# Kernel tuning notes

Measured on AMD Instinct MI355X. Metric: run time of the kernel, lower is better.

The kernel has to match this reference:

```python
import jax, jax.numpy as jnp
import numpy as np

B, T, C, H = 2, 2048, 2048, 16
HS = C // H
EPS = 1e-5


def _ln(x, w, b):
    mu = jnp.mean(x, axis=-1, keepdims=True)
    var = jnp.mean(jnp.square(x - mu), axis=-1, keepdims=True)
    return (x - mu) * jax.lax.rsqrt(var + EPS) * w + b


def setup_inputs() -> dict:
    key = jax.random.key(0)
    ks = jax.random.split(key, 8)
    s = 0.02
    return {
        "x": jax.random.normal(ks[0], (B, T, C), jnp.float32),
        "ln1_w": jnp.ones((C,), jnp.float32),
        "ln1_b": jnp.zeros((C,), jnp.float32),
        "w_qkv": jax.random.normal(ks[1], (C, 3 * C), jnp.float32) * s,
        "b_qkv": jnp.zeros((3 * C,), jnp.float32),
        "w_proj": jax.random.normal(ks[2], (C, C), jnp.float32) * s,
        "b_proj": jnp.zeros((C,), jnp.float32),
        "ln2_w": jnp.ones((C,), jnp.float32),
        "ln2_b": jnp.zeros((C,), jnp.float32),
        "w_fc": jax.random.normal(ks[3], (C, 4 * C), jnp.float32) * s,
        "b_fc": jnp.zeros((4 * C,), jnp.float32),
        "w_fc2": jax.random.normal(ks[4], (4 * C, C), jnp.float32) * s,
        "b_fc2": jnp.zeros((C,), jnp.float32),
    }


def reference(x, ln1_w, ln1_b, w_qkv, b_qkv, w_proj, b_proj,
              ln2_w, ln2_b, w_fc, b_fc, w_fc2, b_fc2):
    # --- attention branch (kv_cache=None -> L=0, burst=False, no padding mask) ---
    h = _ln(x, ln1_w, ln1_b)
    qkv = h @ w_qkv + b_qkv  # (B, T, 3C)
    q, k, v = jnp.split(qkv, 3, axis=-1)
    q = q.reshape(B, T, H, HS).transpose(0, 2, 1, 3)  # (B, H, T, HS)
    k = k.reshape(B, T, H, HS).transpose(0, 2, 1, 3)
    v = v.reshape(B, T, H, HS).transpose(0, 2, 1, 3)
    att = jnp.einsum('bhqd,bhkd->bhqk', q, k) * (1.0 / np.sqrt(HS))
    causal = jnp.tril(jnp.ones((T, T), bool))  # bias[0:T, 0:T]
    att = jnp.where(causal, att, -jnp.inf)
    att = jax.nn.softmax(att, axis=-1)
    y = jnp.einsum('bhqk,bhkd->bhqd', att, v)
    y = y.transpose(0, 2, 1, 3).reshape(B, T, C)
    y = y @ w_proj + b_proj
    x = x + y
    # --- MLP branch ---
    h = _ln(x, ln2_w, ln2_b)
    h = jax.nn.gelu(h @ w_fc + b_fc, approximate=False)
    x = x + (h @ w_fc2 + b_fc2)
    return x
```

## Files before the change

kernel.cpp:

```cpp
#include <hip/hip_runtime.h>
#include <hip/hip_bf16.h>
#include <cstdint>
#include <cstddef>

typedef __attribute__((ext_vector_type(8))) short bf16x8;
typedef __attribute__((ext_vector_type(4))) float f32x4;

#define DEVI __device__ __forceinline__

DEVI unsigned short f2bf(float f) {
  union { float f; unsigned u; } x; x.f = f;
  unsigned r = x.u + 0x7fffu + ((x.u >> 16) & 1u);
  return (unsigned short)(r >> 16);
}

DEVI float exp2fast(float x) {
#if __has_builtin(__builtin_amdgcn_exp2f)
  return __builtin_amdgcn_exp2f(x);
#else
  return exp2f(x);
#endif
}

DEVI void gload_lds16(const void* g, void* l) {
  __builtin_amdgcn_global_load_lds((const __attribute__((address_space(1))) void*)g,
                                   (__attribute__((address_space(3))) void*)l, 16, 0, 0);
}

DEVI f32x4 mfma16(bf16x8 a, bf16x8 b, f32x4 c) {
  return __builtin_amdgcn_mfma_f32_16x16x32_bf16(a, b, c, 0, 0, 0);
}

__global__ __launch_bounds__(256) void transpose_to_bf16(
    const float* __restrict__ w, unsigned short* __restrict__ wt, int K, int N) {
  __shared__ float tile[32][33];
  const int n0 = blockIdx.x * 32, k0 = blockIdx.y * 32;
  const int tx = threadIdx.x, ty = threadIdx.y;
#pragma unroll
  for (int i = 0; i < 4; i++)
    tile[ty + i * 8][tx] = w[(size_t)(k0 + ty + i * 8) * N + n0 + tx];
  __syncthreads();
#pragma unroll
  for (int i = 0; i < 4; i++)
    wt[(size_t)(n0 + ty + i * 8) * K + k0 + tx] = f2bf(tile[tx][ty + i * 8]);
}

__global__ __launch_bounds__(256) void transpose_v(
    const unsigned short* __restrict__ in, unsigned short* __restrict__ out) {
  __shared__ unsigned short tile[32][33];
  const int bh = blockIdx.z;
  const unsigned short* inp = in + (size_t)bh * 2048 * 128;
  unsigned short* op = out + (size_t)bh * 2048 * 128;
  const int t0 = blockIdx.x * 32, d0 = blockIdx.y * 32;
  const int tx = threadIdx.x, ty = threadIdx.y;
#pragma unroll
  for (int i = 0; i < 4; i++)
    tile[ty + i * 8][tx] = inp[(size_t)(t0 + ty + i * 8) * 128 + d0 + tx];
  __syncthreads();
#pragma unroll
  for (int i = 0; i < 4; i++)
    op[(size_t)(d0 + ty + i * 8) * 2048 + t0 + tx] = tile[tx][ty + i * 8];
}

__global__ __launch_bounds__(256) void ln_kernel(
    const float* __restrict__ x, const float* __restrict__ gw,
    const float* __restrict__ gb, unsigned short* __restrict__ out) {
  __shared__ float red[8];
  const int row = blockIdx.x, tid = threadIdx.x;
  const float* xr = x + (size_t)row * 2048;
  f32x4 a = *((const f32x4*)xr + tid * 2);
  f32x4 b = *((const f32x4*)xr + tid * 2 + 1);
  float s = a[0] + a[1] + a[2] + a[3] + b[0] + b[1] + b[2] + b[3];
#pragma unroll
  for (int m = 32; m >= 1; m >>= 1) s += __shfl_xor(s, m, 64);
  if ((tid & 63) == 0) red[tid >> 6] = s;
  __syncthreads();
  const float mu = (red[0] + red[1] + red[2] + red[3]) * (1.f / 2048.f);
  float d[8]; float ss = 0.f;
#pragma unroll
  for (int j = 0; j < 8; j++) {
    float v = ((j < 4) ? a[j] : b[j - 4]) - mu;
    d[j] = v; ss += v * v;
  }
#pragma unroll
  for (int m = 32; m >= 1; m >>= 1) ss += __shfl_xor(ss, m, 64);
  if ((tid & 63) == 0) red[4 + (tid >> 6)] = ss;
  __syncthreads();
  const float var = (red[4] + red[5] + red[6] + red[7]) * (1.f / 2048.f);
  const float rstd = rsqrtf(var + 1e-5f);
  f32x4 w0 = *((const f32x4*)gw + tid * 2), w1 = *((const f32x4*)gw + tid * 2 + 1);
  f32x4 b0 = *((const f32x4*)gb + tid * 2), b1 = *((const f32x4*)gb + tid * 2 + 1);
  union { bf16x8 v; unsigned short u[8]; } o;
#pragma unroll
  for (int j = 0; j < 8; j++) {
    float wv = (j < 4) ? w0[j] : w1[j - 4];
    float bv = (j < 4) ? b0[j] : b1[j - 4];
    o.u[j] = f2bf(d[j] * rstd * wv + bv);
  }
  *(bf16x8*)(out + (size_t)row * 2048 + tid * 8) = o.v;
}

template <int EPI>
DEVI void epilogue_store(float v, int row, int col, int Nn,
                         const float* __restrict__ res, float* __restrict__ outf,
                         unsigned short* __restrict__ outb, unsigned short* __restrict__ oq,
                         unsigned short* __restrict__ ok, unsigned short* __restrict__ ov) {
  if constexpr (EPI == 0) {
    const int which = col >> 11, cc = col & 2047;
    const int hh = cc >> 7, hs = cc & 127;
    const int bb = row >> 11, tt = row & 2047;
    const size_t bh = (size_t)(bb * 16 + hh);
    const unsigned short bits = f2bf(v);
    if (which == 0) oq[(bh * 2048 + tt) * 128 + hs] = bits;
    else if (which == 1) ok[(bh * 2048 + tt) * 128 + hs] = bits;
    else ov[(bh * 2048 + tt) * 128 + hs] = bits;
  } else if constexpr (EPI == 1) {
    const float ge = 0.5f * v * (1.0f + erff(v * 0.70710678118654752f));
    outb[(size_t)row * Nn + col] = f2bf(ge);
  } else {
    outf[(size_t)row * Nn + col] = v + res[(size_t)row * Nn + col];
  }
}

template <int EPI>
__global__ __launch_bounds__(512, 2) void gemm256(
    const unsigned short* __restrict__ A, const unsigned short* __restrict__ Bt,
    const float* __restrict__ bias, const float* __restrict__ res,
    float* __restrict__ outf, unsigned short* __restrict__ outb,
    unsigned short* __restrict__ oq, unsigned short* __restrict__ ok,
    unsigned short* __restrict__ ov, int Nn, int Kk, int nbn) {
  __shared__ unsigned short As[2][256 * 64];
  __shared__ unsigned short Bs[2][256 * 64];
  const int tid = threadIdx.x;
  const int lane = tid & 63, wid = tid >> 6;
  const int i = lane & 15, g = lane >> 4;
  const int wm = wid >> 2, wn = wid & 3;
  const int nwg = gridDim.x;
  const int sid = (blockIdx.x & 7) * (nwg >> 3) + (blockIdx.x >> 3);
  const int m0 = (sid / nbn) * 256, n0 = (sid % nbn) * 256;

  auto stageA = [&](int bf, int kt, int h) {
#pragma unroll
    for (int c = 0; c < 2; c++) {
      const int cb = h * 1024 + c * 512 + wid * 64;
      const int ci = cb + lane;
      const int row = ci >> 3;
      const int kc = (ci & 7) ^ (row & 7);
      gload_lds16(A + (size_t)(m0 + row) * Kk + kt + kc * 8, &As[bf][(size_t)cb * 8]);
    }
  };
  auto stageB = [&](int bf, int kt, int h) {
#pragma unroll
    for (int c = 0; c < 2; c++) {
      const int cb = h * 1024 + c * 512 + wid * 64;
      const int ci = cb + lane;
      const int row = ci >> 3;
      const int kc = (ci & 7) ^ (row & 7);
      gload_lds16(Bt + (size_t)(n0 + row) * Kk + kt + kc * 8, &Bs[bf][(size_t)cb * 8]);
    }
  };
  auto ldA = [&](int bf, int jj, int ks) -> bf16x8 {
    const int row = (2 * jj + wm) * 16 + i;
    return *(const bf16x8*)((const char*)&As[bf][0] + row * 128 + ((((ks << 2) + g) ^ (i & 7)) << 4));
  };
  auto ldB = [&](int bf, int n, int ks) -> bf16x8 {
    const int row = (4 * n + wn) * 16 + i;
    return *(const bf16x8*)((const char*)&Bs[bf][0] + row * 128 + ((((ks << 2) + g) ^ (i & 7)) << 4));
  };

  f32x4 acc[8][4] = {};
  const int NT = Kk >> 6;

  stageA(0, 0, 0);
  stageB(0, 0, 0);
  stageB(0, 0, 1);
  stageA(0, 0, 1);
  asm volatile("s_waitcnt vmcnt(4)" ::: "memory");
  __builtin_amdgcn_s_barrier();
  __builtin_amdgcn_sched_barrier(0);

  bf16x8 a_lo[4][2], a_hi[4][2], b_lo[2][2], b_hi[2][2];
  for (int t = 0; t < NT; ++t) {
    const int cur = t & 1, nxt = cur ^ 1;
    const int ktn = (t + 1) << 6;
    const bool hn = (t + 1) < NT;
#pragma unroll
    for (int n = 0; n < 2; n++) { b_lo[n][0] = ldB(cur, n, 0); b_lo[n][1] = ldB(cur, n, 1); }
#pragma unroll
    for (int jj = 0; jj < 4; jj++) { a_lo[jj][0] = ldA(cur, jj, 0); a_lo[jj][1] = ldA(cur, jj, 1); }
    if (hn) { stageA(nxt, ktn, 0); stageB(nxt, ktn, 0); }
    if (hn) asm volatile("s_waitcnt vmcnt(4)" ::: "memory");
    else    asm volatile("s_waitcnt vmcnt(0)" ::: "memory");
    __builtin_amdgcn_s_barrier();
    __builtin_amdgcn_sched_barrier(0);
    __builtin_amdgcn_s_setprio(1);
#pragma unroll
    for (int jj = 0; jj < 4; jj++)
#pragma unroll
      for (int n = 0; n < 2; n++) {
        acc[jj][n] = mfma16(a_lo[jj][0], b_lo[n][0], acc[jj][n]);
        acc[jj][n] = mfma16(a_lo[jj][1], b_lo[n][1], acc[jj][n]);
      }
    __builtin_amdgcn_s_setprio(0);
#pragma unroll
    for (int n = 0; n < 2; n++) { b_hi[n][0] = ldB(cur, 2 + n, 0); b_hi[n][1] = ldB(cur, 2 + n, 1); }
#pragma unroll
    for (int jj = 0; jj < 4; jj++) { a_hi[jj][0] = ldA(cur, 4 + jj, 0); a_hi[jj][1] = ldA(cur, 4 + jj, 1); }
    if (hn) { stageB(nxt, ktn, 1); stageA(nxt, ktn, 1); }
    if (hn) asm volatile("s_waitcnt vmcnt(4)" ::: "memory");
    __builtin_amdgcn_s_barrier();
    __builtin_amdgcn_sched_barrier(0);
    __builtin_amdgcn_s_setprio(1);
#pragma unroll
    for (int jj = 0; jj < 4; jj++)
#pragma unroll
      for (int n = 0; n < 2; n++) {
        acc[jj][2 + n] = mfma16(a_lo[jj][0], b_hi[n][0], acc[jj][2 + n]);
        acc[jj][2 + n] = mfma16(a_lo[jj][1], b_hi[n][1], acc[jj][2 + n]);
      }
#pragma unroll
    for (int jj = 0; jj < 4; jj++)
#pragma unroll
      for (int n = 0; n < 2; n++) {
        acc[4 + jj][n] = mfma16(a_hi[jj][0], b_lo[n][0], acc[4 + jj][n]);
        acc[4 + jj][n] = mfma16(a_hi[jj][1], b_lo[n][1], acc[4 + jj][n]);
      }
#pragma unroll
    for (int jj = 0; jj < 4; jj++)
#pragma unroll
      for (int n = 0; n < 2; n++) {
        acc[4 + jj][2 + n] = mfma16(a_hi[jj][0], b_hi[n][0], acc[4 + jj][2 + n]);
        acc[4 + jj][2 + n] = mfma16(a_hi[jj][1], b_hi[n][1], acc[4 + jj][2 + n]);
      }
    __builtin_amdgcn_s_setprio(0);
  }

#pragma unroll
  for (int jj = 0; jj < 8; jj++)
#pragma unroll
    for (int n = 0; n < 4; n++) {
      const int col = n0 + (4 * n + wn) * 16 + i;
      const float bv = bias[col];
#pragma unroll
      for (int r = 0; r < 4; r++) {
        const int row = m0 + (2 * jj + wm) * 16 + g * 4 + r;
        epilogue_store<EPI>(acc[jj][n][r] + bv, row, col, Nn, res, outf, outb, oq, ok, ov);
      }
    }
}

template <int EPI>
__global__ __launch_bounds__(512, 2) void gemm128(
    const unsigned short* __restrict__ A, const unsigned short* __restrict__ Bt,
    const float* __restrict__ bias, const float* __restrict__ res,
    float* __restrict__ outf, unsigned short* __restrict__ outb,
    unsigned short* __restrict__ oq, unsigned short* __restrict__ ok,
    unsigned short* __restrict__ ov, int Nn, int Kk, int nbn) {
  __shared__ unsigned short As[2][128 * 64];
  __shared__ unsigned short Bs[2][256 * 64];
  const int tid = threadIdx.x;
  const int lane = tid & 63, wid = tid >> 6;
  const int i = lane & 15, g = lane >> 4;
  const int wm = wid >> 2, wn = wid & 3;
  const int nwg = gridDim.x;
  const int sid = (blockIdx.x & 7) * (nwg >> 3) + (blockIdx.x >> 3);
  const int m0 = (sid / nbn) * 128, n0 = (sid % nbn) * 256;

  auto stageA = [&](int bf, int kt) {
#pragma unroll
    for (int c = 0; c < 2; c++) {
      const int cb = c * 512 + wid * 64;
      const int ci = cb + lane;
      const int row = ci >> 3;
      const int kc = (ci & 7) ^ (row & 7);
      gload_lds16(A + (size_t)(m0 + row) * Kk + kt + kc * 8, &As[bf][(size_t)cb * 8]);
    }
  };
  auto stageB = [&](int bf, int kt, int h) {
#pragma unroll
    for (int c = 0; c < 2; c++) {
      const int cb = h * 1024 + c * 512 + wid * 64;
      const int ci = cb + lane;
      const int row = ci >> 3;
      const int kc = (ci & 7) ^ (row & 7);
      gload_lds16(Bt + (size_t)(n0 + row) * Kk + kt + kc * 8, &Bs[bf][(size_t)cb * 8]);
    }
  };
  auto ldA = [&](int bf, int jj, int ks) -> bf16x8 {
    const int row = (2 * jj + wm) * 16 + i;
    return *(const bf16x8*)((const char*)&As[bf][0] + row * 128 + ((((ks << 2) + g) ^ (i & 7)) << 4));
  };
  auto ldB = [&](int bf, int n, int ks) -> bf16x8 {
    const int row = (4 * n + wn) * 16 + i;
    return *(const bf16x8*)((const char*)&Bs[bf][0] + row * 128 + ((((ks << 2) + g) ^ (i & 7)) << 4));
  };

  f32x4 acc[4][4] = {};
  const int NT = Kk >> 6;

  stageA(0, 0);
  stageB(0, 0, 0);
  stageB(0, 0, 1);
  asm volatile("s_waitcnt vmcnt(2)" ::: "memory");
  __builtin_amdgcn_s_barrier();
  __builtin_amdgcn_sched_barrier(0);

  bf16x8 af[4][2], b_lo[2][2], b_hi[2][2];
  for (int t = 0; t < NT; ++t) {
    const int cur = t & 1, nxt = cur ^ 1;
    const int ktn = (t + 1) << 6;
    const bool hn = (t + 1) < NT;
#pragma unroll
    for (int n = 0; n < 2; n++) { b_lo[n][0] = ldB(cur, n, 0); b_lo[n][1] = ldB(cur, n, 1); }
#pragma unroll
    for (int jj = 0; jj < 4; jj++) { af[jj][0] = ldA(cur, jj, 0); af[jj][1] = ldA(cur, jj, 1); }
    if (hn) { stageA(nxt, ktn); stageB(nxt, ktn, 0); }
    if (hn) asm volatile("s_waitcnt vmcnt(4)" ::: "memory");
    else    asm volatile("s_waitcnt vmcnt(0)" ::: "memory");
    __builtin_amdgcn_s_barrier();
    __builtin_amdgcn_sched_barrier(0);
    __builtin_amdgcn_s_setprio(1);
#pragma unroll
    for (int jj = 0; jj < 4; jj++)
#pragma unroll
      for (int n = 0; n < 2; n++) {
        acc[jj][n] = mfma16(af[jj][0], b_lo[n][0], acc[jj][n]);
        acc[jj][n] = mfma16(af[jj][1], b_lo[n][1], acc[jj][n]);
      }
    __builtin_amdgcn_s_setprio(0);
#pragma unroll
    for (int n = 0; n < 2; n++) { b_hi[n][0] = ldB(cur, 2 + n, 0); b_hi[n][1] = ldB(cur, 2 + n, 1); }
    if (hn) stageB(nxt, ktn, 1);
    if (hn) asm volatile("s_waitcnt vmcnt(2)" ::: "memory");
    __builtin_amdgcn_s_barrier();
    __builtin_amdgcn_sched_barrier(0);
    __builtin_amdgcn_s_setprio(1);
#pragma unroll
    for (int jj = 0; jj < 4; jj++)
#pragma unroll
      for (int n = 0; n < 2; n++) {
        acc[jj][2 + n] = mfma16(af[jj][0], b_hi[n][0], acc[jj][2 + n]);
        acc[jj][2 + n] = mfma16(af[jj][1], b_hi[n][1], acc[jj][2 + n]);
      }
    __builtin_amdgcn_s_setprio(0);
  }

#pragma unroll
  for (int jj = 0; jj < 4; jj++)
#pragma unroll
    for (int n = 0; n < 4; n++) {
      const int col = n0 + (4 * n + wn) * 16 + i;
      const float bv = bias[col];
#pragma unroll
      for (int r = 0; r < 4; r++) {
        const int row = m0 + (2 * jj + wm) * 16 + g * 4 + r;
        epilogue_store<EPI>(acc[jj][n][r] + bv, row, col, Nn, res, outf, outb, oq, ok, ov);
      }
    }
}

__global__ __launch_bounds__(256) void attn_kernel(
    const unsigned short* __restrict__ q, const unsigned short* __restrict__ k,
    const unsigned short* __restrict__ vt, unsigned short* __restrict__ y) {
  __shared__ unsigned short Ks[64 * 128];
  __shared__ unsigned short Vs[128 * 64];
  __shared__ unsigned short Ps[4][16 * 64];
  const int tid = threadIdx.x, lane = tid & 63, w = tid >> 6;
  const int i = lane & 15, g = lane >> 4;
  const int p = blockIdx.x, bh = blockIdx.y;
  const int q0A = p * 64, q0B = (31 - p) * 64;
  const int tB = 31 - p;
  const size_t hb = (size_t)bh * (2048 * 128);
  const float sc2 = 0.08838834764831845f * 1.44269504088896341f;

  bf16x8 qfA[4], qfB[4];
  {
    const int qra = q0A + w * 16 + i, qrb = q0B + w * 16 + i;
#pragma unroll
    for (int kc = 0; kc < 4; kc++) {
      qfA[kc] = *(const bf16x8*)(q + hb + (size_t)qra * 128 + kc * 32 + g * 8);
      qfB[kc] = *(const bf16x8*)(q + hb + (size_t)qrb * 128 + kc * 32 + g * 8);
    }
  }
  f32x4 oA[8] = {}, oB[8] = {};
  float mA = -__builtin_inff(), lA = 0.f, mB = -__builtin_inff(), lB = 0.f;

  auto proc = [&](const bf16x8 (&qf)[4], f32x4 (&oacc)[8], float& mrun, float& lrun,
                  bool diag) {
    f32x4 st[4];
#pragma unroll
    for (int ct = 0; ct < 4; ct++) {
      f32x4 a = {};
      const int kvr = ct * 16 + i;
#pragma unroll
      for (int kc = 0; kc < 4; kc++) {
        bf16x8 kf = *(const bf16x8*)((char*)Ks + kvr * 256 + (((kc * 4 + g) ^ (i & 7)) << 4));
        a = mfma16(kf, qf[kc], a);
      }
      st[ct] = a;
    }
    float tm = -__builtin_inff();
    const int ql = w * 16 + i;
#pragma unroll
    for (int ct = 0; ct < 4; ct++)
#pragma unroll
      for (int r = 0; r < 4; r++) {
        float v = st[ct][r] * sc2;
        if (diag) {
          const int kvl = ct * 16 + g * 4 + r;
          if (kvl > ql) v = -__builtin_inff();
        }
        st[ct][r] = v;
        tm = fmaxf(tm, v);
      }
    tm = fmaxf(tm, __shfl_xor(tm, 16, 64));
    tm = fmaxf(tm, __shfl_xor(tm, 32, 64));
    if (!__all(tm - mrun <= 8.f)) {
      const float mnew = fmaxf(mrun, tm);
      const float al = exp2fast(mrun - mnew);
      float ar[4];
#pragma unroll
      for (int r = 0; r < 4; r++) ar[r] = __shfl(al, g * 4 + r, 64);
#pragma unroll
      for (int dt = 0; dt < 8; dt++)
#pragma unroll
        for (int r = 0; r < 4; r++) oacc[dt][r] *= ar[r];
      lrun *= al;
      mrun = mnew;
    }
    float ps = 0.f;
#pragma unroll
    for (int ct = 0; ct < 4; ct++)
#pragma unroll
      for (int r = 0; r < 4; r++) {
        const float pv = exp2fast(st[ct][r] - mrun);
        st[ct][r] = pv;
        ps += pv;
      }
    ps += __shfl_xor(ps, 16, 64);
    ps += __shfl_xor(ps, 32, 64);
    lrun += ps;
#pragma unroll
    for (int ct = 0; ct < 4; ct++) {
      unsigned w0, w1;
      asm("v_cvt_pk_bf16_f32 %0, %1, %2" : "=v"(w0) : "v"(st[ct][0]), "v"(st[ct][1]));
      asm("v_cvt_pk_bf16_f32 %0, %1, %2" : "=v"(w1) : "v"(st[ct][2]), "v"(st[ct][3]));
      char* pb = (char*)&Ps[w][0] + i * 128 +
                 ((((2 * ct + (g >> 1)) ^ (i & 7)) << 4) + (g & 1) * 8);
      *(uint2*)pb = make_uint2(w0, w1);
    }
    bf16x8 pf[2];
#pragma unroll
    for (int kvc = 0; kvc < 2; kvc++)
      pf[kvc] = *(const bf16x8*)((char*)&Ps[w][0] + i * 128 + (((kvc * 4 + g) ^ (i & 7)) << 4));
#pragma unroll
    for (int dt = 0; dt < 8; dt++) {
      const int dr = dt * 16 + i;
#pragma unroll
      for (int kvc = 0; kvc < 2; kvc++) {
        bf16x8 vf = *(const bf16x8*)((char*)Vs + dr * 128 + (((kvc * 4 + g) ^ (dr & 7)) << 4));
        oacc[dt] = mfma16(pf[kvc], vf, oacc[dt]);
      }
    }
  };

  for (int t = 0; t <= tB; ++t) {
    const int j0 = t * 64;
    __syncthreads();
#pragma unroll
    for (int it = 0; it < 4; it++) {
      const int ci = it * 256 + tid;
      const int kv = ci >> 4, ccl = ci & 15;
      gload_lds16(k + hb + (size_t)(j0 + kv) * 128 + ((ccl ^ (kv & 7)) << 3),
                  (char*)Ks + (size_t)(it * 256 + w * 64) * 16);
      const int dd = ci >> 3, c2l = ci & 7;
      gload_lds16(vt + hb + (size_t)dd * 2048 + j0 + ((c2l ^ (dd & 7)) << 3),
                  (char*)Vs + (size_t)(it * 256 + w * 64) * 16);
    }
    __syncthreads();
    if (t <= p) proc(qfA, oA, mA, lA, t == p);
    proc(qfB, oB, mB, lB, t == tB);
  }

  const int bb = bh >> 4, hh = bh & 15;
  auto finish = [&](const f32x4 (&oacc)[8], float lrun, int q0s) {
    const float inv_i = 1.f / lrun;
    float ir[4];
#pragma unroll
    for (int r = 0; r < 4; r++) ir[r] = __shfl(inv_i, g * 4 + r, 64);
#pragma unroll
    for (int r = 0; r < 4; r++) {
      const int row = q0s + w * 16 + g * 4 + r;
#pragma unroll
      for (int dt = 0; dt < 8; dt++) {
        const int d = dt * 16 + i;
        y[((size_t)(bb * 2048 + row)) * 2048 + hh * 128 + d] = f2bf(oacc[dt][r] * ir[r]);
      }
    }
  };
  finish(oA, lA, q0A);
  finish(oB, lB, q0B);
}

extern "C" void kernel_launch(void* const* d_in, const int* in_sizes, int n_in,
                              void* d_out, int out_size, void* d_ws, size_t ws_size,
                              hipStream_t stream) {
  const float* x      = (const float*)d_in[0];
  const float* ln1_w  = (const float*)d_in[1];
  const float* ln1_b  = (const float*)d_in[2];
  const float* w_qkv  = (const float*)d_in[3];
  const float* b_qkv  = (const float*)d_in[4];
  const float* w_proj = (const float*)d_in[5];
  const float* b_proj = (const float*)d_in[6];
  const float* ln2_w  = (const float*)d_in[7];
  const float* ln2_b  = (const float*)d_in[8];
  const float* w_fc   = (const float*)d_in[9];
  const float* b_fc   = (const float*)d_in[10];
  const float* w_fc2  = (const float*)d_in[11];
  const float* b_fc2  = (const float*)d_in[12];

  char* ws = (char*)d_ws;
  unsigned short* wt_qkv  = (unsigned short*)(ws + 0);
  unsigned short* wt_proj = (unsigned short*)(ws + 25165824);
  unsigned short* qb      = (unsigned short*)(ws + 33554432);
  unsigned short* kb      = (unsigned short*)(ws + 50331648);
  unsigned short* wt_fc   = (unsigned short*)(ws + 67108864);
  unsigned short* wt_fc2  = (unsigned short*)(ws + 100663296);
  unsigned short* hb      = (unsigned short*)(ws + 134217728);
  unsigned short* vtb     = (unsigned short*)(ws + 150994944);
  unsigned short* yb      = (unsigned short*)(ws + 167772160);
  float*          x1      = (float*)(ws + 184549376);
  unsigned short* hfc     = (unsigned short*)(ws + 0);
  float* outp = (float*)d_out;

  dim3 tb(32, 8);
  transpose_to_bf16<<<dim3(6144 / 32, 2048 / 32), tb, 0, stream>>>(w_qkv, wt_qkv, 2048, 6144);
  transpose_to_bf16<<<dim3(2048 / 32, 2048 / 32), tb, 0, stream>>>(w_proj, wt_proj, 2048, 2048);
  transpose_to_bf16<<<dim3(8192 / 32, 2048 / 32), tb, 0, stream>>>(w_fc, wt_fc, 2048, 8192);
  transpose_to_bf16<<<dim3(2048 / 32, 8192 / 32), tb, 0, stream>>>(w_fc2, wt_fc2, 8192, 2048);

  ln_kernel<<<4096, 256, 0, stream>>>(x, ln1_w, ln1_b, hb);

  gemm128<0><<<768, 512, 0, stream>>>(
      hb, wt_qkv, b_qkv, nullptr, nullptr, nullptr, qb, kb, yb, 6144, 2048, 24);
  transpose_v<<<dim3(2048 / 32, 128 / 32, 32), tb, 0, stream>>>(yb, vtb);

  attn_kernel<<<dim3(16, 32), 256, 0, stream>>>(qb, kb, vtb, yb);

  gemm128<2><<<256, 512, 0, stream>>>(
      yb, wt_proj, b_proj, x, x1, nullptr, nullptr, nullptr, nullptr, 2048, 2048, 8);

  ln_kernel<<<4096, 256, 0, stream>>>(x1, ln2_w, ln2_b, hb);

  gemm256<1><<<512, 512, 0, stream>>>(
      hb, wt_fc, b_fc, nullptr, nullptr, hfc, nullptr, nullptr, nullptr, 8192, 2048, 32);

  gemm128<2><<<256, 512, 0, stream>>>(
      hfc, wt_fc2, b_fc2, x1, outp, nullptr, nullptr, nullptr, nullptr, 2048, 8192, 8);
}
```

Measured before the change: 661.7 us.

## Software-pipeline GEMM main loop with cross-iteration LDS fragment prefetch

Restructures the double-buffered GEMM K-loop so the low-half A/B fragments for the next tile are read from LDS at the end of the current iteration. The low-half global-to-LDS stage for tile t+2 is issued into the buffer just freed, and the first MFMA block starts without waiting on a barrier. This aims to overlap LDS reads and global loads with MFMA work and remove one barrier stall per iteration. It relies on careful vmcnt accounting and buffer reuse, which could race if the counts are wrong.

```diff
diff --git a/kernel.cpp b/kernel.cpp
--- a/kernel.cpp
+++ b/kernel.cpp
@@ -175,22 +175,44 @@
   stageB(0, 0, 0);
   stageB(0, 0, 1);
   stageA(0, 0, 1);
-  asm volatile("s_waitcnt vmcnt(4)" ::: "memory");
+  if (NT > 1) {
+    stageB(1, 64, 0);
+    stageA(1, 64, 0);
+    asm volatile("s_waitcnt vmcnt(4)" ::: "memory");
+  } else {
+    asm volatile("s_waitcnt vmcnt(0)" ::: "memory");
+  }
   __builtin_amdgcn_s_barrier();
   __builtin_amdgcn_sched_barrier(0);
 
   bf16x8 a_lo[4][2], a_hi[4][2], b_lo[2][2], b_hi[2][2];
+#pragma unroll
+  for (int n = 0; n < 2; n++) { b_lo[n][0] = ldB(0, n, 0); b_lo[n][1] = ldB(0, n, 1); }
+#pragma unroll
+  for (int jj = 0; jj < 4; jj++) { a_lo[jj][0] = ldA(0, jj, 0); a_lo[jj][1] = ldA(0, jj, 1); }
+
   for (int t = 0; t < NT; ++t) {
     const int cur = t & 1, nxt = cur ^ 1;
-    const int ktn = (t + 1) << 6;
-    const bool hn = (t + 1) < NT;
-#pragma unroll
-    for (int n = 0; n < 2; n++) { b_lo[n][0] = ldB(cur, n, 0); b_lo[n][1] = ldB(cur, n, 1); }
-#pragma unroll
-    for (int jj = 0; jj < 4; jj++) { a_lo[jj][0] = ldA(cur, jj, 0); a_lo[jj][1] = ldA(cur, jj, 1); }
-    if (hn) { stageA(nxt, ktn, 0); stageB(nxt, ktn, 0); }
-    if (hn) asm volatile("s_waitcnt vmcnt(4)" ::: "memory");
-    else    asm volatile("s_waitcnt vmcnt(0)" ::: "memory");
+    const int ktn = (t + 1) << 6, kt2 = (t + 2) << 6;
+    const bool hn = (t + 1) < NT, hn2 = (t + 2) < NT;
+    __builtin_amdgcn_s_setprio(1);
+#pragma unroll
+    for (int jj = 0; jj < 4; jj++)
+#pragma unroll
+      for (int n = 0; n < 2; n++) {
+        acc[jj][n] = mfma16(a_lo[jj][0], b_lo[n][0], acc[jj][n]);
+        acc[jj][n] = mfma16(a_lo[jj][1], b_lo[n][1], acc[jj][n]);
+      }
+    __builtin_amdgcn_s_setprio(0);
+#pragma unroll
+    for (int n = 0; n < 2; n++) { b_hi[n][0] = ldB(cur, 2 + n, 0); b_hi[n][1] = ldB(cur, 2 + n, 1); }
+#pragma unroll
+    for (int jj = 0; jj < 4; jj++) { a_hi[jj][0] = ldA(cur, 4 + jj, 0); a_hi[jj][1] = ldA(cur, 4 + jj, 1); }
+    if (hn) {
+      stageB(nxt, ktn, 1);
+      stageA(nxt, ktn, 1);
+      asm volatile("s_waitcnt vmcnt(4)" ::: "memory");
+    }
     __builtin_amdgcn_s_barrier();
     __builtin_amdgcn_sched_barrier(0);
     __builtin_amdgcn_s_setprio(1);
@@ -198,23 +220,6 @@
     for (int jj = 0; jj < 4; jj++)
 #pragma unroll
       for (int n = 0; n < 2; n++) {
-        acc[jj][n] = mfma16(a_lo[jj][0], b_lo[n][0], acc[jj][n]);
-        acc[jj][n] = mfma16(a_lo[jj][1], b_lo[n][1], acc[jj][n]);
-      }
-    __builtin_amdgcn_s_setprio(0);
-#pragma unroll
-    for (int n = 0; n < 2; n++) { b_hi[n][0] = ldB(cur, 2 + n, 0); b_hi[n][1] = ldB(cur, 2 + n, 1); }
-#pragma unroll
-    for (int jj = 0; jj < 4; jj++) { a_hi[jj][0] = ldA(cur, 4 + jj, 0); a_hi[jj][1] = ldA(cur, 4 + jj, 1); }
-    if (hn) { stageB(nxt, ktn, 1); stageA(nxt, ktn, 1); }
-    if (hn) asm volatile("s_waitcnt vmcnt(4)" ::: "memory");
-    __builtin_amdgcn_s_barrier();
-    __builtin_amdgcn_sched_barrier(0);
-    __builtin_amdgcn_s_setprio(1);
-#pragma unroll
-    for (int jj = 0; jj < 4; jj++)
-#pragma unroll
-      for (int n = 0; n < 2; n++) {
         acc[jj][2 + n] = mfma16(a_lo[jj][0], b_hi[n][0], acc[jj][2 + n]);
         acc[jj][2 + n] = mfma16(a_lo[jj][1], b_hi[n][1], acc[jj][2 + n]);
       }
@@ -233,6 +238,23 @@
         acc[4 + jj][2 + n] = mfma16(a_hi[jj][1], b_hi[n][1], acc[4 + jj][2 + n]);
       }
     __builtin_amdgcn_s_setprio(0);
+    if (hn) {
+#pragma unroll
+      for (int n = 0; n < 2; n++) { b_lo[n][0] = ldB(nxt, n, 0); b_lo[n][1] = ldB(nxt, n, 1); }
+#pragma unroll
+      for (int jj = 0; jj < 4; jj++) { a_lo[jj][0] = ldA(nxt, jj, 0); a_lo[jj][1] = ldA(nxt, jj, 1); }
+    }
+    if (hn2) {
+      stageB(cur, kt2, 0);
+      stageA(cur, kt2, 0);
+      asm volatile("s_waitcnt vmcnt(4)" ::: "memory");
+    } else if (hn) {
+      asm volatile("s_waitcnt vmcnt(0)" ::: "memory");
+    }
+    if (hn) {
+      __builtin_amdgcn_s_barrier();
+      __builtin_amdgcn_sched_barrier(0);
+    }
   }
 
 #pragma unroll
```

Result: no change. 671.8 us (+1.5%).

## Deepen gemm256 prefetch to two k-tiles ahead with finer-grained phased stores

Applied to the files above, without the earlier changes.

Restructures the 256x256 GEMM main loop so global-to-LDS loads for tile t+2 are issued into the current buffer halves once their fragments have been read, keeping more loads in flight. The loop is split into four MFMA phases separated by barriers and lgkmcnt waits, with staged halves interleaved between phases. This aims to hide global memory latency better, at the cost of many more workgroup barriers per iteration and tighter correctness dependencies on the buffer-reuse ordering.

```diff
diff --git a/kernel.cpp b/kernel.cpp
--- a/kernel.cpp
+++ b/kernel.cpp
@@ -122,6 +122,9 @@
   }
 }
 
+#define BAR() do { __builtin_amdgcn_s_barrier(); __builtin_amdgcn_sched_barrier(0); } while (0)
+#define LGKM0() do { asm volatile("s_waitcnt lgkmcnt(0)" ::: "memory"); __builtin_amdgcn_sched_barrier(0); } while (0)
+
 template <int EPI>
 __global__ __launch_bounds__(512, 2) void gemm256(
     const unsigned short* __restrict__ A, const unsigned short* __restrict__ Bt,
@@ -171,28 +174,33 @@
   f32x4 acc[8][4] = {};
   const int NT = Kk >> 6;
 
+  stageB(0, 0, 0);
   stageA(0, 0, 0);
-  stageB(0, 0, 0);
   stageB(0, 0, 1);
   stageA(0, 0, 1);
-  asm volatile("s_waitcnt vmcnt(4)" ::: "memory");
-  __builtin_amdgcn_s_barrier();
-  __builtin_amdgcn_sched_barrier(0);
+  if (NT > 1) {
+    asm volatile("s_waitcnt vmcnt(4)" ::: "memory");
+    stageB(1, 64, 0);
+    stageA(1, 64, 0);
+    stageB(1, 64, 1);
+    asm volatile("s_waitcnt vmcnt(6)" ::: "memory");
+  } else {
+    asm volatile("s_waitcnt vmcnt(0)" ::: "memory");
+  }
+  BAR();
 
   bf16x8 a_lo[4][2], a_hi[4][2], b_lo[2][2], b_hi[2][2];
   for (int t = 0; t < NT; ++t) {
     const int cur = t & 1, nxt = cur ^ 1;
-    const int ktn = (t + 1) << 6;
-    const bool hn = (t + 1) < NT;
+    const int kt1 = (t + 1) << 6, kt2 = (t + 2) << 6;
+    const bool h1 = (t + 1) < NT, h2 = (t + 2) < NT;
 #pragma unroll
     for (int n = 0; n < 2; n++) { b_lo[n][0] = ldB(cur, n, 0); b_lo[n][1] = ldB(cur, n, 1); }
 #pragma unroll
     for (int jj = 0; jj < 4; jj++) { a_lo[jj][0] = ldA(cur, jj, 0); a_lo[jj][1] = ldA(cur, jj, 1); }
-    if (hn) { stageA(nxt, ktn, 0); stageB(nxt, ktn, 0); }
-    if (hn) asm volatile("s_waitcnt vmcnt(4)" ::: "memory");
-    else    asm volatile("s_waitcnt vmcnt(0)" ::: "memory");
-    __builtin_amdgcn_s_barrier();
-    __builtin_amdgcn_sched_barrier(0);
+    if (h1) stageA(nxt, kt1, 1);
+    BAR();
+    LGKM0();
     __builtin_amdgcn_s_setprio(1);
 #pragma unroll
     for (int jj = 0; jj < 4; jj++)
@@ -202,14 +210,12 @@
         acc[jj][n] = mfma16(a_lo[jj][1], b_lo[n][1], acc[jj][n]);
       }
     __builtin_amdgcn_s_setprio(0);
+    BAR();
 #pragma unroll
     for (int n = 0; n < 2; n++) { b_hi[n][0] = ldB(cur, 2 + n, 0); b_hi[n][1] = ldB(cur, 2 + n, 1); }
-#pragma unroll
-    for (int jj = 0; jj < 4; jj++) { a_hi[jj][0] = ldA(cur, 4 + jj, 0); a_hi[jj][1] = ldA(cur, 4 + jj, 1); }
-    if (hn) { stageB(nxt, ktn, 1); stageA(nxt, ktn, 1); }
-    if (hn) asm volatile("s_waitcnt vmcnt(4)" ::: "memory");
-    __builtin_amdgcn_s_barrier();
-    __builtin_amdgcn_sched_barrier(0);
+    if (h2) stageB(cur, kt2, 0);
+    BAR();
+    LGKM0();
     __builtin_amdgcn_s_setprio(1);
 #pragma unroll
     for (int jj = 0; jj < 4; jj++)
@@ -218,6 +224,14 @@
         acc[jj][2 + n] = mfma16(a_lo[jj][0], b_hi[n][0], acc[jj][2 + n]);
         acc[jj][2 + n] = mfma16(a_lo[jj][1], b_hi[n][1], acc[jj][2 + n]);
       }
+    __builtin_amdgcn_s_setprio(0);
+    BAR();
+#pragma unroll
+    for (int jj = 0; jj < 4; jj++) { a_hi[jj][0] = ldA(cur, 4 + jj, 0); a_hi[jj][1] = ldA(cur, 4 + jj, 1); }
+    if (h2) stageA(cur, kt2, 0);
+    BAR();
+    LGKM0();
+    __builtin_amdgcn_s_setprio(1);
 #pragma unroll
     for (int jj = 0; jj < 4; jj++)
 #pragma unroll
@@ -225,6 +239,16 @@
         acc[4 + jj][n] = mfma16(a_hi[jj][0], b_lo[n][0], acc[4 + jj][n]);
         acc[4 + jj][n] = mfma16(a_hi[jj][1], b_lo[n][1], acc[4 + jj][n]);
       }
+    __builtin_amdgcn_s_setprio(0);
+    BAR();
+    if (h2) {
+      stageB(cur, kt2, 1);
+      asm volatile("s_waitcnt vmcnt(6)" ::: "memory");
+    } else if (h1) {
+      asm volatile("s_waitcnt vmcnt(0)" ::: "memory");
+    }
+    BAR();
+    __builtin_amdgcn_s_setprio(1);
 #pragma unroll
     for (int jj = 0; jj < 4; jj++)
 #pragma unroll
@@ -233,6 +257,7 @@
         acc[4 + jj][2 + n] = mfma16(a_hi[jj][1], b_hi[n][1], acc[4 + jj][2 + n]);
       }
     __builtin_amdgcn_s_setprio(0);
+    BAR();
   }
 
 #pragma unroll
```

Result: no change. 673.8 us (+1.8%).
